# Performance work log

Hardware: AMD Instinct MI355X
Metric: run time of the kernel (lower is better)

The kernel has to match this reference:

```python
import jax, jax.numpy as jnp
import numpy as np

SCALE = 1.0  # alpha / rank = 32 / 32


def setup_inputs() -> dict:
    key = jax.random.key(0)
    k_x, k_w, k_b, k_a, k_bb = jax.random.split(key, 5)
    B, S, D = 4, 4096, 3072
    depth, rank = 4, 32
    x = jax.random.normal(k_x, (B, S, D), dtype=jnp.float32)
    W = jax.random.normal(k_w, (D, D), dtype=jnp.float32) * (1.0 / np.sqrt(D))
    b = jax.random.normal(k_b, (D,), dtype=jnp.float32) * 0.02
    lora_A = jax.random.normal(k_a, (depth, rank, D), dtype=jnp.float32) * (1.0 / np.sqrt(D))
    lora_B = jax.random.normal(k_bb, (depth, D, rank), dtype=jnp.float32) * 0.02
    return {"x": x, "W": W, "b": b, "lora_A": lora_A, "lora_B": lora_B}


def reference(x, W, b, lora_A, lora_B):
    # base: y = x @ W.T + b
    base_out = jnp.einsum('bsi,oi->bso', x, W) + b
    # stacked LoRA: sum_d (x @ A_d.T @ B_d.T); dropout=0 -> identity
    # down-project to rank per depth: [B,S,depth,rank]
    z = jnp.einsum('bsi,dri->bsdr', x, lora_A)
    lora_out = jnp.einsum('bsdr,dor->bso', z, lora_B)
    return base_out + lora_out * SCALE
```

## Files before the change

### kernel.cpp

```cpp
#include <hip/hip_runtime.h>
#include <hip/hip_bf16.h>


typedef unsigned short ushort_t;
typedef short bf16x8 __attribute__((ext_vector_type(8)));
typedef float floatx4 __attribute__((ext_vector_type(4)));
typedef unsigned short ushortx4 __attribute__((ext_vector_type(4)));

__device__ __forceinline__ ushort_t f2bf(float f) {
    __hip_bfloat16 h = __float2bfloat16(f);
    return *(ushort_t*)&h;
}

__device__ __forceinline__ void async_load16(const void* g, void* l) {
    __builtin_amdgcn_global_load_lds(
        (const __attribute__((address_space(1))) void*)g,
        (__attribute__((address_space(3))) void*)l,
        16, 0, 0);
}

__global__ __launch_bounds__(256)
void cvt_kernel(const float* __restrict__ in, ushort_t* __restrict__ out, int n4) {
    int i = blockIdx.x * 256 + threadIdx.x;
    if (i < n4) {
        const float4 v = ((const float4*)in)[i];
        ushortx4 o = { f2bf(v.x), f2bf(v.y), f2bf(v.z), f2bf(v.w) };
        ((ushortx4*)out)[i] = o;
    }
}

__global__ __launch_bounds__(256)
void transpose_loraB_kernel(const float* __restrict__ lb,
                            ushort_t* __restrict__ out) {
    int idx = blockIdx.x * 256 + threadIdx.x;
    int n = idx >> 7;
    int j = idx & 127;
    int d = j >> 5, r = j & 31;
    out[idx] = f2bf(lb[(size_t)d * (3072 * 32) + (size_t)n * 32 + r]);
}

template <int KT1, int KT2, bool OUT_F32>
__global__ __launch_bounds__(256)
void gemm_bt_kernel(const ushort_t* __restrict__ A, int lda,
                    const ushort_t* __restrict__ B, int ldb,
                    const ushort_t* __restrict__ A2,
                    const ushort_t* __restrict__ B2,
                    const float* __restrict__ bias,
                    void* __restrict__ Cv, int ldc)
{
    __shared__ ushort_t As[128 * 32];
    __shared__ ushort_t Bs[128 * 32];

    const int t    = threadIdx.x;
    const int lane = t & 63;
    const int wave = t >> 6;
    const int wr   = wave >> 1, wc = wave & 1;
    const int quad = lane >> 4, l16 = lane & 15;

    const int mBase = blockIdx.y * 128;
    const int nBase = blockIdx.x * 128;

    floatx4 acc[4][4] = {};

    const int c0 = t,        r0 = c0 >> 2, col0 = (c0 & 3) << 3;
    const int c1 = t + 256,  r1 = c1 >> 2, col1 = (c1 & 3) << 3;

    for (int kt = 0; kt < KT1 + KT2; ++kt) {
        const ushort_t* ap; const ushort_t* bp; int la, lb_, ko;
        if (kt < KT1) { ap = A;  la = lda; bp = B;  lb_ = ldb; ko = kt * 32; }
        else          { ap = A2; la = 128; bp = B2; lb_ = 128; ko = (kt - KT1) * 32; }

        async_load16(ap + (size_t)(mBase + r0) * la + ko + col0, &As[c0 * 8]);
        async_load16(ap + (size_t)(mBase + r1) * la + ko + col1, &As[c1 * 8]);
        async_load16(bp + (size_t)(nBase + r0) * lb_ + ko + col0, &Bs[c0 * 8]);
        async_load16(bp + (size_t)(nBase + r1) * lb_ + ko + col1, &Bs[c1 * 8]);

        __syncthreads();

        bf16x8 af[4], bf[4];
#pragma unroll
        for (int mi = 0; mi < 4; ++mi)
            af[mi] = *(const bf16x8*)&As[(wr * 64 + mi * 16 + l16) * 32 + quad * 8];
#pragma unroll
        for (int ni = 0; ni < 4; ++ni)
            bf[ni] = *(const bf16x8*)&Bs[(wc * 64 + ni * 16 + l16) * 32 + quad * 8];

#pragma unroll
        for (int mi = 0; mi < 4; ++mi)
#pragma unroll
            for (int ni = 0; ni < 4; ++ni)
                acc[mi][ni] = __builtin_amdgcn_mfma_f32_16x16x32_bf16(
                    af[mi], bf[ni], acc[mi][ni], 0, 0, 0);

        __syncthreads();
    }

#pragma unroll
    for (int ni = 0; ni < 4; ++ni) {
        const int col = nBase + wc * 64 + ni * 16 + l16;
        const float bv = bias ? bias[col] : 0.0f;
#pragma unroll
        for (int mi = 0; mi < 4; ++mi) {
            const int row = mBase + wr * 64 + mi * 16 + quad * 4;
#pragma unroll
            for (int r = 0; r < 4; ++r) {
                const float v = acc[mi][ni][r] + bv;
                if (OUT_F32) {
                    ((float*)Cv)[(size_t)(row + r) * ldc + col] = v;
                } else {
                    ((ushort_t*)Cv)[(size_t)(row + r) * ldc + col] = f2bf(v);
                }
            }
        }
    }
}

extern "C" void kernel_launch(void* const* d_in, const int* in_sizes, int n_in,
                              void* d_out, int out_size, void* d_ws, size_t ws_size,
                              hipStream_t stream) {
    const float* x  = (const float*)d_in[0];
    const float* W  = (const float*)d_in[1];
    const float* b  = (const float*)d_in[2];
    const float* lA = (const float*)d_in[3];
    const float* lB = (const float*)d_in[4];
    float* out = (float*)d_out;

    constexpr int M = 4 * 4096;
    constexpr int N = 3072;
    constexpr int K = 3072;
    constexpr size_t nX  = (size_t)M * K;
    constexpr size_t nW  = (size_t)N * K;
    constexpr size_t nLA = (size_t)128 * K;
    constexpr size_t nLB = (size_t)128 * N;

    ushort_t* xb  = (ushort_t*)d_ws;
    ushort_t* Wb  = xb  + nX;
    ushort_t* lAb = Wb  + nW;
    ushort_t* Bp  = lAb + nLA;
    ushort_t* z   = Bp  + nLB;

    cvt_kernel<<<nX  / 4 / 256, 256, 0, stream>>>(x,  xb,  (int)(nX  / 4));
    cvt_kernel<<<nW  / 4 / 256, 256, 0, stream>>>(W,  Wb,  (int)(nW  / 4));
    cvt_kernel<<<nLA / 4 / 256, 256, 0, stream>>>(lA, lAb, (int)(nLA / 4));

    transpose_loraB_kernel<<<nLB / 256, 256, 0, stream>>>(lB, Bp);

    gemm_bt_kernel<96, 0, false><<<dim3(1, M / 128), 256, 0, stream>>>(
        xb, K, lAb, K, nullptr, nullptr, nullptr, z, 128);

    gemm_bt_kernel<96, 4, true><<<dim3(N / 128, M / 128), 256, 0, stream>>>(
        xb, K, Wb, K, z, Bp, b, out, N);
}
```

Before: 780.5 us.

## Fold LoRA into an effective weight matrix and swizzle LDS tiles

Computes W_eff = W + B_cat·A_cat with a small GEMM (rank 128, K=128) that writes a bf16 merged weight. This removes the separate x·A down-projection GEMM over the full activation, the x·A intermediate, and the extra K steps in the main GEMM. It also XOR-swizzles the LDS tile layout to reduce bank conflicts on fragment reads. The trade-off is a slightly different rounding order, since the LoRA product is now added to W in fp32 and then rounded to bf16.

```diff
diff --git a/kernel.cpp b/kernel.cpp
--- a/kernel.cpp
+++ b/kernel.cpp
@@ -39,12 +39,20 @@
     out[idx] = f2bf(lb[(size_t)d * (3072 * 32) + (size_t)n * 32 + r]);
 }
 
-template <int KT1, int KT2, bool OUT_F32>
+__global__ __launch_bounds__(256)
+void transpose_loraA_kernel(const float* __restrict__ la,
+                            ushort_t* __restrict__ out) {
+    int idx = blockIdx.x * 256 + threadIdx.x;
+    int kk = idx >> 7;
+    int j  = idx & 127;
+    out[idx] = f2bf(la[(size_t)j * 3072 + kk]);
+}
+
+template <int KT, bool OUT_F32, bool ADD_MAT>
 __global__ __launch_bounds__(256)
 void gemm_bt_kernel(const ushort_t* __restrict__ A, int lda,
                     const ushort_t* __restrict__ B, int ldb,
-                    const ushort_t* __restrict__ A2,
-                    const ushort_t* __restrict__ B2,
+                    const float* __restrict__ Cadd,
                     const float* __restrict__ bias,
                     void* __restrict__ Cv, int ldc)
 {
@@ -62,28 +70,28 @@
 
     floatx4 acc[4][4] = {};
 
-    const int c0 = t,        r0 = c0 >> 2, col0 = (c0 & 3) << 3;
-    const int c1 = t + 256,  r1 = c1 >> 2, col1 = (c1 & 3) << 3;
+    const int p0 = t,       r0 = p0 >> 2, g0 = ((p0 & 3) ^ ((r0 >> 1) & 3)) << 3;
+    const int p1 = t + 256, r1 = p1 >> 2, g1 = ((p1 & 3) ^ ((r1 >> 1) & 3)) << 3;
 
-    for (int kt = 0; kt < KT1 + KT2; ++kt) {
-        const ushort_t* ap; const ushort_t* bp; int la, lb_, ko;
-        if (kt < KT1) { ap = A;  la = lda; bp = B;  lb_ = ldb; ko = kt * 32; }
-        else          { ap = A2; la = 128; bp = B2; lb_ = 128; ko = (kt - KT1) * 32; }
+    const int qs = (quad ^ ((l16 >> 1) & 3)) << 3;
 
-        async_load16(ap + (size_t)(mBase + r0) * la + ko + col0, &As[c0 * 8]);
-        async_load16(ap + (size_t)(mBase + r1) * la + ko + col1, &As[c1 * 8]);
-        async_load16(bp + (size_t)(nBase + r0) * lb_ + ko + col0, &Bs[c0 * 8]);
-        async_load16(bp + (size_t)(nBase + r1) * lb_ + ko + col1, &Bs[c1 * 8]);
+    for (int kt = 0; kt < KT; ++kt) {
+        const int ko = kt * 32;
+
+        async_load16(A + (size_t)(mBase + r0) * lda + ko + g0, &As[p0 * 8]);
+        async_load16(A + (size_t)(mBase + r1) * lda + ko + g1, &As[p1 * 8]);
+        async_load16(B + (size_t)(nBase + r0) * ldb + ko + g0, &Bs[p0 * 8]);
+        async_load16(B + (size_t)(nBase + r1) * ldb + ko + g1, &Bs[p1 * 8]);
 
         __syncthreads();
 
         bf16x8 af[4], bf[4];
 #pragma unroll
         for (int mi = 0; mi < 4; ++mi)
-            af[mi] = *(const bf16x8*)&As[(wr * 64 + mi * 16 + l16) * 32 + quad * 8];
+            af[mi] = *(const bf16x8*)&As[(wr * 64 + mi * 16 + l16) * 32 + qs];
 #pragma unroll
         for (int ni = 0; ni < 4; ++ni)
-            bf[ni] = *(const bf16x8*)&Bs[(wc * 64 + ni * 16 + l16) * 32 + quad * 8];
+            bf[ni] = *(const bf16x8*)&Bs[(wc * 64 + ni * 16 + l16) * 32 + qs];
 
 #pragma unroll
         for (int mi = 0; mi < 4; ++mi)
@@ -104,7 +112,8 @@
             const int row = mBase + wr * 64 + mi * 16 + quad * 4;
 #pragma unroll
             for (int r = 0; r < 4; ++r) {
-                const float v = acc[mi][ni][r] + bv;
+                float v = acc[mi][ni][r] + bv;
+                if (ADD_MAT) v += Cadd[(size_t)(row + r) * ldc + col];
                 if (OUT_F32) {
                     ((float*)Cv)[(size_t)(row + r) * ldc + col] = v;
                 } else {
@@ -130,24 +139,21 @@
     constexpr int K = 3072;
     constexpr size_t nX  = (size_t)M * K;
     constexpr size_t nW  = (size_t)N * K;
-    constexpr size_t nLA = (size_t)128 * K;
-    constexpr size_t nLB = (size_t)128 * N;
+    constexpr size_t nT  = (size_t)128 * K;
 
-    ushort_t* xb  = (ushort_t*)d_ws;
-    ushort_t* Wb  = xb  + nX;
-    ushort_t* lAb = Wb  + nW;
-    ushort_t* Bp  = lAb + nLA;
-    ushort_t* z   = Bp  + nLB;
+    ushort_t* xb    = (ushort_t*)d_ws;
+    ushort_t* Weffb = xb + nX;
+    ushort_t* Bp    = Weffb + nW;
+    ushort_t* At    = Bp + nT;
 
-    cvt_kernel<<<nX  / 4 / 256, 256, 0, stream>>>(x,  xb,  (int)(nX  / 4));
-    cvt_kernel<<<nW  / 4 / 256, 256, 0, stream>>>(W,  Wb,  (int)(nW  / 4));
-    cvt_kernel<<<nLA / 4 / 256, 256, 0, stream>>>(lA, lAb, (int)(nLA / 4));
+    cvt_kernel<<<nX / 4 / 256, 256, 0, stream>>>(x, xb, (int)(nX / 4));
 
-    transpose_loraB_kernel<<<nLB / 256, 256, 0, stream>>>(lB, Bp);
+    transpose_loraB_kernel<<<nT / 256, 256, 0, stream>>>(lB, Bp);
+    transpose_loraA_kernel<<<nT / 256, 256, 0, stream>>>(lA, At);
 
-    gemm_bt_kernel<96, 0, false><<<dim3(1, M / 128), 256, 0, stream>>>(
-        xb, K, lAb, K, nullptr, nullptr, nullptr, z, 128);
+    gemm_bt_kernel<4, false, true><<<dim3(N / 128, N / 128), 256, 0, stream>>>(
+        Bp, 128, At, 128, W, nullptr, Weffb, N);
 
-    gemm_bt_kernel<96, 4, true><<<dim3(N / 128, M / 128), 256, 0, stream>>>(
-        xb, K, Wb, K, z, Bp, b, out, N);
+    gemm_bt_kernel<96, true, false><<<dim3(N / 128, M / 128), 256, 0, stream>>>(
+        xb, K, Weffb, K, nullptr, b, out, N);
 }
```

Result: faster. 723.4 us (-7.3%).
